# Optimization experiments

Measured on AMD Instinct MI355X. Metric: run time of the kernel, lower is better.

The kernel has to match this reference:

```python
import jax, jax.numpy as jnp
import numpy as np

B, S, D = 2, 2048, 1024
H = 16
HD = D // H  # 64


def setup_inputs() -> dict:
    key = jax.random.key(0)
    ks = jax.random.split(key, 6)
    sc = 1.0 / np.sqrt(D)
    x = jax.random.normal(ks[0], (B, S, D), dtype=jnp.float32)
    Wq = jax.random.normal(ks[1], (D, D), dtype=jnp.float32) * sc
    Wk = jax.random.normal(ks[2], (D, D), dtype=jnp.float32) * sc
    Wv = jax.random.normal(ks[3], (D, D), dtype=jnp.float32) * sc
    Wo = jax.random.normal(ks[4], (D, D), dtype=jnp.float32) * sc
    bo = jax.random.normal(ks[5], (D,), dtype=jnp.float32) * 0.01
    return {"x": x, "Wq": Wq, "Wk": Wk, "Wv": Wv, "Wo": Wo, "bo": bo}


def reference(x, Wq, Wk, Wv, Wo, bo):
    # projections: [B,S,D] -> [B,H,S,HD]
    def split_heads(t):
        return t.reshape(B, S, H, HD).transpose(0, 2, 1, 3)

    q = split_heads(x @ Wq)
    k = split_heads(x @ Wk)
    v = split_heads(x @ Wv)

    # naive full score matrix [B,H,S,S], masked causal, scaled softmax
    scores = jnp.einsum("bhqd,bhkd->bhqk", q, k)
    causal = jnp.tril(jnp.ones((S, S), dtype=bool))  # True = keep
    scores = jnp.where(causal, scores, -jnp.inf)
    attn = jax.nn.softmax(scores / np.sqrt(HD), axis=-1)

    ctx = jnp.einsum("bhqk,bhkd->bhqd", attn, v)  # [B,H,S,HD]
    ctx = ctx.transpose(0, 2, 1, 3).reshape(B, S, D)
    return ctx @ Wo + bo
```

## Files before the change

### kernel.cpp

```cpp
#include <hip/hip_runtime.h>

#define BB 2
#define SS 2048
#define DD 1024
#define HH 16
#define HD 64
#define MM (BB*SS)

typedef __bf16 bf16x8 __attribute__((ext_vector_type(8)));
typedef short  s16x4  __attribute__((ext_vector_type(4)));
typedef float  f32x4  __attribute__((ext_vector_type(4)));

#ifndef __has_builtin
#define __has_builtin(x) 0
#endif

__device__ __forceinline__ unsigned short f2bf(float f) {
    unsigned int u = __float_as_uint(f);
    u = (u + 0x7fffu + ((u >> 16) & 1u)) >> 16;
    return (unsigned short)u;
}
__device__ __forceinline__ unsigned int pack2(float a, float b) {
    return (unsigned int)f2bf(a) | ((unsigned int)f2bf(b) << 16);
}
__device__ __forceinline__ unsigned int pack2_fast(float a, float b) {
#if __has_builtin(__builtin_amdgcn_perm)
    return __builtin_amdgcn_perm(__float_as_uint(b) + 0x8000u,
                                 __float_as_uint(a) + 0x8000u, 0x07060302u);
#else
    return ((__float_as_uint(a) + 0x8000u) >> 16) |
           ((__float_as_uint(b) + 0x8000u) & 0xffff0000u);
#endif
}

__device__ __forceinline__ void gload_lds16(const unsigned short* g, unsigned short* l) {
    __builtin_amdgcn_global_load_lds(
        (const __attribute__((address_space(1))) void*)g,
        (__attribute__((address_space(3))) void*)l, 16, 0, 0);
}

__global__ __launch_bounds__(256) void prep_kernel(const float* __restrict__ x,
                                                   const float* __restrict__ Wq,
                                                   const float* __restrict__ Wk,
                                                   const float* __restrict__ Wv,
                                                   const float* __restrict__ Wo,
                                                   unsigned short* __restrict__ Xb,
                                                   unsigned short* __restrict__ Wqkvt,
                                                   unsigned short* __restrict__ Wot) {
    __shared__ float tile[32][33];
    const int bx = blockIdx.x;
    const int t = threadIdx.x;
    if (bx < 2048) {
        int gid = bx * 256 + t;
        int i = gid * 8;
        float4 a = *(const float4*)(x + i);
        float4 b = *(const float4*)(x + i + 4);
        uint4 o;
        o.x = pack2(a.x, a.y); o.y = pack2(a.z, a.w);
        o.z = pack2(b.x, b.y); o.w = pack2(b.z, b.w);
        ((uint4*)Xb)[gid] = o;
        return;
    }
    int pb = bx - 2048;
    int p = pb >> 10, rem = pb & 1023;
    int bxx = rem & 31, byy = rem >> 5;
    const float* src = (p == 0) ? Wq : (p == 1) ? Wk : (p == 2) ? Wv : Wo;
    unsigned short* dst = (p == 3) ? Wot : (Wqkvt + (size_t)p * DD * DD);
    int tx = t & 31, ty = t >> 5;
    int n = bxx * 32 + tx;
#pragma unroll
    for (int i = 0; i < 4; ++i) {
        int k = byy * 32 + ty + i * 8;
        tile[ty + i * 8][tx] = src[k * DD + n];
    }
    __syncthreads();
#pragma unroll
    for (int i = 0; i < 4; ++i) {
        int n2 = bxx * 32 + ty + i * 8;
        int k2 = byy * 32 + tx;
        dst[n2 * DD + k2] = f2bf(tile[tx][ty + i * 8]);
    }
}

#define GEMM_K_LOOP(Aglob, Bglob)                                                 \
    __shared__ unsigned short smem[128 * 132];                                    \
    unsigned short (*As)[64]  = (unsigned short(*)[64])smem;                      \
    unsigned short (*Bs)[64]  = (unsigned short(*)[64])(smem + 128 * 64);         \
    unsigned short (*Es)[132] = (unsigned short(*)[132])smem;                     \
    const int n0 = blockIdx.x * 128, m0 = blockIdx.y * 128;                       \
    const int t = threadIdx.x;                                                    \
    const int wave = t >> 6, lane = t & 63;                                       \
    const int wm = wave >> 1, wn = wave & 1;                                      \
    const int l15 = lane & 15, quad = lane >> 4;                                  \
    const int lr = lane >> 3, lg = (lane & 7);                                    \
    const int lc = (lg ^ lr) * 8;                    \
    f32x4 acc[4][4];                                                              \
    _Pragma("unroll") for (int i = 0; i < 4; ++i)                                 \
        _Pragma("unroll") for (int j = 0; j < 4; ++j) acc[i][j] = f32x4{0,0,0,0}; \
    for (int kt = 0; kt < 16; ++kt) {                                             \
        if (kt) __syncthreads();                                                  \
        _Pragma("unroll") for (int i = 0; i < 4; ++i) {                           \
            int row = wave * 32 + i * 8;                                          \
            gload_lds16(Aglob + (size_t)(m0 + row + lr) * DD + kt * 64 + lc, &As[row][0]); \
            gload_lds16(Bglob + (size_t)(n0 + row + lr) * DD + kt * 64 + lc, &Bs[row][0]); \
        }                                                                         \
        __syncthreads();                                                          \
        _Pragma("unroll") for (int kh = 0; kh < 2; ++kh) {                        \
            bf16x8 af[4], bfr[4];                                                 \
            _Pragma("unroll") for (int s = 0; s < 4; ++s)                         \
                af[s] = *(const bf16x8*)&As[wm * 64 + s * 16 + l15][((kh * 4 + quad) ^ (l15 & 7)) * 8]; \
            _Pragma("unroll") for (int s = 0; s < 4; ++s)                         \
                bfr[s] = *(const bf16x8*)&Bs[wn * 64 + s * 16 + l15][((kh * 4 + quad) ^ (l15 & 7)) * 8]; \
            _Pragma("unroll") for (int i = 0; i < 4; ++i)                         \
                _Pragma("unroll") for (int j = 0; j < 4; ++j)                     \
                    acc[i][j] = __builtin_amdgcn_mfma_f32_16x16x32_bf16(af[i], bfr[j], acc[i][j], 0, 0, 0); \
        }                                                                         \
    }                                                                             \
    __syncthreads();

__global__ __launch_bounds__(256) void qkv_gemm_kernel(const unsigned short* __restrict__ Xb,
                                                       const unsigned short* __restrict__ Wt,
                                                       unsigned short* __restrict__ Qg,
                                                       unsigned short* __restrict__ Kg,
                                                       unsigned short* __restrict__ Vt) {
    GEMM_K_LOOP(Xb, Wt)
    const int p = n0 >> 10;
    const float qs = (p == 0) ? 0.18033688011112042f : 1.0f;
    if (p < 2) {
#pragma unroll
        for (int sm = 0; sm < 4; ++sm)
#pragma unroll
            for (int sn = 0; sn < 4; ++sn)
#pragma unroll
                for (int i = 0; i < 4; ++i)
                    Es[wm * 64 + sm * 16 + quad * 4 + i][wn * 64 + sn * 16 + l15] = f2bf(acc[sm][sn][i] * qs);
    } else {
#pragma unroll
        for (int sm = 0; sm < 4; ++sm)
#pragma unroll
            for (int sn = 0; sn < 4; ++sn)
#pragma unroll
                for (int i = 0; i < 4; ++i)
                    Es[wn * 64 + sn * 16 + l15][wm * 64 + sm * 16 + quad * 4 + i] = f2bf(acc[sm][sn][i]);
    }
    __syncthreads();
    const int h0 = (n0 & 1023) >> 6;
    if (p < 2) {
        unsigned short* dst0 = p ? Kg : Qg;
        int ml = t >> 1, seg = t & 1;
        int gm = m0 + ml, b = gm >> 11, s = gm & 2047;
        unsigned short* dptr = dst0 + ((size_t)(b * HH + h0 + seg) * SS + s) * HD;
#pragma unroll
        for (int j = 0; j < 8; ++j)
            *(uint4*)(dptr + j * 8) = *(const uint4*)&Es[ml][seg * 64 + j * 8];
    } else {
        int nl = t >> 1, mh = t & 1;
        int h = h0 + (nl >> 6), hd = nl & 63;
        int b = m0 >> 11, s0 = (m0 & 2047) + mh * 64;
        unsigned short* dptr = Vt + ((size_t)(b * HH + h) * HD + hd) * SS + s0;
#pragma unroll
        for (int j = 0; j < 8; ++j)
            *(uint4*)(dptr + j * 8) = *(const uint4*)&Es[nl][mh * 64 + j * 8];
    }
}

__global__ __launch_bounds__(256) void out_gemm_kernel(const unsigned short* __restrict__ Ctxb,
                                                       const unsigned short* __restrict__ Wot,
                                                       const float* __restrict__ bo,
                                                       float* __restrict__ out) {
    GEMM_K_LOOP(Ctxb, Wot)
    (void)Es;
#pragma unroll
    for (int sn = 0; sn < 4; ++sn) {
        int gn = n0 + wn * 64 + sn * 16 + l15;
        float bias = bo[gn];
#pragma unroll
        for (int sm = 0; sm < 4; ++sm)
#pragma unroll
            for (int i = 0; i < 4; ++i) {
                int gm = m0 + wm * 64 + sm * 16 + quad * 4 + i;
                out[(size_t)gm * DD + gn] = acc[sm][sn][i] + bias;
            }
    }
}

__global__ __launch_bounds__(256) void attn_kernel(const unsigned short* __restrict__ Qg,
                                                   const unsigned short* __restrict__ Kg,
                                                   const unsigned short* __restrict__ Vt,
                                                   unsigned short* __restrict__ Ctxb) {
    __shared__ unsigned short Ks[2][128][64];
    __shared__ unsigned short Vs[2][64][128];

    const int bh = blockIdx.x;
    const int qt = (int)gridDim.y - 1 - (int)blockIdx.y;
    const int t = threadIdx.x;
    const int wave = t >> 6, lane = t & 63;
    const int l15 = lane & 15, quad = lane >> 4;
    const int q0 = qt * 64;
    const int qmax = q0 + 63;
    const int b = bh >> 4, h = bh & 15;

    const unsigned short* Qb = Qg + (size_t)bh * SS * HD;
    const unsigned short* Kb = Kg + (size_t)bh * SS * HD;
    const unsigned short* Vb = Vt + (size_t)bh * HD * SS;

    const int qrow = q0 + wave * 16 + l15;
    bf16x8 bq[2];
#pragma unroll
    for (int hh = 0; hh < 2; ++hh)
        bq[hh] = *(const bf16x8*)(Qb + (size_t)qrow * HD + hh * 32 + quad * 8);

    const int rloc = lane >> 3, pcl = lane & 7;
    const int vrl = lane >> 4, vgc = lane & 15;
    const unsigned short* ksrc[4];
    const unsigned short* vsrc[4];
#pragma unroll
    for (int j = 0; j < 4; ++j) {
        int krow = (wave * 4 + j) * 8 + rloc;
        ksrc[j] = Kb + (size_t)krow * HD + (pcl ^ rloc) * 8;
        int vrow = wave * 16 + j * 4 + vrl;
        vsrc[j] = Vb + (size_t)vrow * SS + (vgc ^ (vrow & 15)) * 8;
    }

    f32x4 acc[4] = {f32x4{0,0,0,0}, f32x4{0,0,0,0}, f32x4{0,0,0,0}, f32x4{0,0,0,0}};
    float l = 0.f;
    const int nkt = (qmax >> 7) + 1;

#pragma unroll
    for (int j = 0; j < 4; ++j) {
        gload_lds16(ksrc[j], &Ks[0][(wave * 4 + j) * 8][0]);
        gload_lds16(vsrc[j], &Vs[0][wave * 16 + j * 4][0]);
    }
    __syncthreads();

    for (int kt = 0; kt < nkt; ++kt) {
        const int buf = kt & 1;
        const int k0 = kt * 128;
        if (kt + 1 < nkt) {
            const int nb = buf ^ 1;
#pragma unroll
            for (int j = 0; j < 4; ++j) {
                gload_lds16(ksrc[j] + (size_t)(kt + 1) * 128 * HD, &Ks[nb][(wave * 4 + j) * 8][0]);
                gload_lds16(vsrc[j] + (kt + 1) * 128,              &Vs[nb][wave * 16 + j * 4][0]);
            }
        }

        auto tile_body = [&](int kbmax, bool tail) {
#pragma unroll
            for (int kb = 0; kb < 8; ++kb) {
                if (kb >= kbmax) continue;
                f32x4 St = f32x4{0, 0, 0, 0};
#pragma unroll
                for (int hh = 0; hh < 2; ++hh) {
                    bf16x8 ak = *(const bf16x8*)&Ks[buf][kb * 16 + l15][((hh * 4 + quad) ^ (l15 & 7)) * 8];
                    St = __builtin_amdgcn_mfma_f32_16x16x32_bf16(ak, bq[hh], St, 0, 0, 0);
                }
                if (tail) {
#pragma unroll
                    for (int r = 0; r < 4; ++r)
                        if (k0 + kb * 16 + quad * 4 + r > qrow) St[r] = -1e30f;
                }
                float e0 = __builtin_amdgcn_exp2f(St[0]);
                float e1 = __builtin_amdgcn_exp2f(St[1]);
                float e2 = __builtin_amdgcn_exp2f(St[2]);
                float e3 = __builtin_amdgcn_exp2f(St[3]);
                l += (e0 + e1) + (e2 + e3);
                uint2 uu;
                uu.x = pack2_fast(e0, e1);
                uu.y = pack2_fast(e2, e3);
                s16x4 ap = *(s16x4*)&uu;
#pragma unroll
                for (int db = 0; db < 4; ++db) {
                    const int pg = (2 * kb + (quad >> 1)) ^ l15;
                    s16x4 bv = *(const s16x4*)&Vs[buf][db * 16 + l15][pg * 8 + (quad & 1) * 4];
                    acc[db] = __builtin_amdgcn_mfma_f32_16x16x16bf16_1k(ap, bv, acc[db], 0, 0, 0);
                }
            }
        };
        if (kt == nkt - 1) tile_body(((qmax - k0) >> 4) + 1, true);
        else               tile_body(8, false);

        __syncthreads();
    }

    l += __shfl_xor(l, 16, 64);
    l += __shfl_xor(l, 32, 64);
    float linv = 1.0f / l;
#pragma unroll
    for (int r = 0; r < 4; ++r) {
        float ir = __shfl(linv, quad * 4 + r, 64);
        int gq = q0 + wave * 16 + quad * 4 + r;
        size_t base = ((size_t)(b * SS + gq)) * DD + h * HD;
#pragma unroll
        for (int db = 0; db < 4; ++db)
            Ctxb[base + db * 16 + l15] = f2bf(acc[db][r] * ir);
    }
}

extern "C" void kernel_launch(void* const* d_in, const int* in_sizes, int n_in,
                              void* d_out, int out_size, void* d_ws, size_t ws_size,
                              hipStream_t stream) {
    const float* x  = (const float*)d_in[0];
    const float* Wq = (const float*)d_in[1];
    const float* Wk = (const float*)d_in[2];
    const float* Wv = (const float*)d_in[3];
    const float* Wo = (const float*)d_in[4];
    const float* bo = (const float*)d_in[5];
    float* out = (float*)d_out;

    char* w = (char*)d_ws;
    unsigned short* Xb    = (unsigned short*)(w);
    unsigned short* Wqkvt = (unsigned short*)(w + (size_t)(8 << 20));
    unsigned short* Wot   = (unsigned short*)(w + (size_t)(14 << 20));
    unsigned short* Qg    = (unsigned short*)(w + (size_t)(16 << 20));
    unsigned short* Kg    = (unsigned short*)(w + (size_t)(24 << 20));
    unsigned short* Vt    = (unsigned short*)(w + (size_t)(32 << 20));
    unsigned short* Ctxb  = (unsigned short*)(w + (size_t)(40 << 20));

    prep_kernel<<<6144, 256, 0, stream>>>(x, Wq, Wk, Wv, Wo, Xb, Wqkvt, Wot);
    qkv_gemm_kernel<<<dim3(3 * DD / 128, MM / 128), 256, 0, stream>>>(Xb, Wqkvt, Qg, Kg, Vt);
    attn_kernel<<<dim3(BB * HH, SS / 64), 256, 0, stream>>>(Qg, Kg, Vt, Ctxb);
    out_gemm_kernel<<<dim3(DD / 128, MM / 128), 256, 0, stream>>>(Ctxb, Wot, bo, out);
}
```

Measured before the change: 174.1 us.

## Double query rows per attention block and compute row sums via MFMA

Each attention block now handles 128 query rows instead of 64, with every wave processing two 16-row query fragments that share each loaded K and V fragment from LDS. This halves K/V global-to-LDS traffic per query and amortizes the LDS reads. The softmax denominator is now accumulated with an MFMA against a ones vector instead of scalar adds plus cross-lane shuffles. In exchange the grid is halved, which reduces parallelism, and the diagonal tile no longer skips fully masked sub-blocks. Register pressure also rises.

```diff
diff --git a/kernel.cpp b/kernel.cpp
--- a/kernel.cpp
+++ b/kernel.cpp
@@ -196,19 +196,22 @@
     const int t = threadIdx.x;
     const int wave = t >> 6, lane = t & 63;
     const int l15 = lane & 15, quad = lane >> 4;
-    const int q0 = qt * 64;
-    const int qmax = q0 + 63;
+    const int q0 = qt * 128;
     const int b = bh >> 4, h = bh & 15;
 
     const unsigned short* Qb = Qg + (size_t)bh * SS * HD;
     const unsigned short* Kb = Kg + (size_t)bh * SS * HD;
     const unsigned short* Vb = Vt + (size_t)bh * HD * SS;
 
-    const int qrow = q0 + wave * 16 + l15;
-    bf16x8 bq[2];
-#pragma unroll
-    for (int hh = 0; hh < 2; ++hh)
-        bq[hh] = *(const bf16x8*)(Qb + (size_t)qrow * HD + hh * 32 + quad * 8);
+    int qrow[2];
+    bf16x8 bq[2][2];
+#pragma unroll
+    for (int qf = 0; qf < 2; ++qf) {
+        qrow[qf] = q0 + wave * 32 + qf * 16 + l15;
+#pragma unroll
+        for (int hh = 0; hh < 2; ++hh)
+            bq[qf][hh] = *(const bf16x8*)(Qb + (size_t)qrow[qf] * HD + hh * 32 + quad * 8);
+    }
 
     const int rloc = lane >> 3, pcl = lane & 7;
     const int vrl = lane >> 4, vgc = lane & 15;
@@ -222,9 +225,14 @@
         vsrc[j] = Vb + (size_t)vrow * SS + (vgc ^ (vrow & 15)) * 8;
     }
 
-    f32x4 acc[4] = {f32x4{0,0,0,0}, f32x4{0,0,0,0}, f32x4{0,0,0,0}, f32x4{0,0,0,0}};
-    float l = 0.f;
-    const int nkt = (qmax >> 7) + 1;
+    f32x4 acc[2][4];
+#pragma unroll
+    for (int qf = 0; qf < 2; ++qf)
+#pragma unroll
+        for (int db = 0; db < 4; ++db) acc[qf][db] = f32x4{0,0,0,0};
+    f32x4 accl[2] = {f32x4{0,0,0,0}, f32x4{0,0,0,0}};
+    const s16x4 ones = {(short)0x3F80, (short)0x3F80, (short)0x3F80, (short)0x3F80};
+    const int nkt = qt + 1;
 
 #pragma unroll
     for (int j = 0; j < 4; ++j) {
@@ -245,55 +253,60 @@
             }
         }
 
-        auto tile_body = [&](int kbmax, bool tail) {
-#pragma unroll
-            for (int kb = 0; kb < 8; ++kb) {
-                if (kb >= kbmax) continue;
-                f32x4 St = f32x4{0, 0, 0, 0};
-#pragma unroll
-                for (int hh = 0; hh < 2; ++hh) {
-                    bf16x8 ak = *(const bf16x8*)&Ks[buf][kb * 16 + l15][((hh * 4 + quad) ^ (l15 & 7)) * 8];
-                    St = __builtin_amdgcn_mfma_f32_16x16x32_bf16(ak, bq[hh], St, 0, 0, 0);
-                }
-                if (tail) {
+        const bool tail = (kt == nkt - 1);
+#pragma unroll
+        for (int kb = 0; kb < 8; ++kb) {
+            f32x4 St[2] = {f32x4{0,0,0,0}, f32x4{0,0,0,0}};
+#pragma unroll
+            for (int hh = 0; hh < 2; ++hh) {
+                bf16x8 ak = *(const bf16x8*)&Ks[buf][kb * 16 + l15][((hh * 4 + quad) ^ (l15 & 7)) * 8];
+                St[0] = __builtin_amdgcn_mfma_f32_16x16x32_bf16(ak, bq[0][hh], St[0], 0, 0, 0);
+                St[1] = __builtin_amdgcn_mfma_f32_16x16x32_bf16(ak, bq[1][hh], St[1], 0, 0, 0);
+            }
+            if (tail) {
+#pragma unroll
+                for (int qf = 0; qf < 2; ++qf)
 #pragma unroll
                     for (int r = 0; r < 4; ++r)
-                        if (k0 + kb * 16 + quad * 4 + r > qrow) St[r] = -1e30f;
-                }
-                float e0 = __builtin_amdgcn_exp2f(St[0]);
-                float e1 = __builtin_amdgcn_exp2f(St[1]);
-                float e2 = __builtin_amdgcn_exp2f(St[2]);
-                float e3 = __builtin_amdgcn_exp2f(St[3]);
-                l += (e0 + e1) + (e2 + e3);
+                        if (k0 + kb * 16 + quad * 4 + r > qrow[qf]) St[qf][r] = -1e30f;
+            }
+            s16x4 ap[2];
+#pragma unroll
+            for (int qf = 0; qf < 2; ++qf) {
+                float e0 = __builtin_amdgcn_exp2f(St[qf][0]);
+                float e1 = __builtin_amdgcn_exp2f(St[qf][1]);
+                float e2 = __builtin_amdgcn_exp2f(St[qf][2]);
+                float e3 = __builtin_amdgcn_exp2f(St[qf][3]);
                 uint2 uu;
                 uu.x = pack2_fast(e0, e1);
                 uu.y = pack2_fast(e2, e3);
-                s16x4 ap = *(s16x4*)&uu;
-#pragma unroll
-                for (int db = 0; db < 4; ++db) {
-                    const int pg = (2 * kb + (quad >> 1)) ^ l15;
-                    s16x4 bv = *(const s16x4*)&Vs[buf][db * 16 + l15][pg * 8 + (quad & 1) * 4];
-                    acc[db] = __builtin_amdgcn_mfma_f32_16x16x16bf16_1k(ap, bv, acc[db], 0, 0, 0);
-                }
-            }
-        };
-        if (kt == nkt - 1) tile_body(((qmax - k0) >> 4) + 1, true);
-        else               tile_body(8, false);
+                ap[qf] = *(s16x4*)&uu;
+            }
+#pragma unroll
+            for (int db = 0; db < 4; ++db) {
+                const int pg = (2 * kb + (quad >> 1)) ^ l15;
+                s16x4 bv = *(const s16x4*)&Vs[buf][db * 16 + l15][pg * 8 + (quad & 1) * 4];
+                acc[0][db] = __builtin_amdgcn_mfma_f32_16x16x16bf16_1k(ap[0], bv, acc[0][db], 0, 0, 0);
+                acc[1][db] = __builtin_amdgcn_mfma_f32_16x16x16bf16_1k(ap[1], bv, acc[1][db], 0, 0, 0);
+            }
+            accl[0] = __builtin_amdgcn_mfma_f32_16x16x16bf16_1k(ap[0], ones, accl[0], 0, 0, 0);
+            accl[1] = __builtin_amdgcn_mfma_f32_16x16x16bf16_1k(ap[1], ones, accl[1], 0, 0, 0);
+        }
 
         __syncthreads();
     }
 
-    l += __shfl_xor(l, 16, 64);
-    l += __shfl_xor(l, 32, 64);
-    float linv = 1.0f / l;
-#pragma unroll
-    for (int r = 0; r < 4; ++r) {
-        float ir = __shfl(linv, quad * 4 + r, 64);
-        int gq = q0 + wave * 16 + quad * 4 + r;
-        size_t base = ((size_t)(b * SS + gq)) * DD + h * HD;
-#pragma unroll
-        for (int db = 0; db < 4; ++db)
-            Ctxb[base + db * 16 + l15] = f2bf(acc[db][r] * ir);
+#pragma unroll
+    for (int qf = 0; qf < 2; ++qf) {
+#pragma unroll
+        for (int r = 0; r < 4; ++r) {
+            float ir = 1.0f / accl[qf][r];
+            int gq = q0 + wave * 32 + qf * 16 + quad * 4 + r;
+            size_t base = ((size_t)(b * SS + gq)) * DD + h * HD;
+#pragma unroll
+            for (int db = 0; db < 4; ++db)
+                Ctxb[base + db * 16 + l15] = f2bf(acc[qf][db][r] * ir);
+        }
     }
 }
 
@@ -319,6 +332,6 @@
 
     prep_kernel<<<6144, 256, 0, stream>>>(x, Wq, Wk, Wv, Wo, Xb, Wqkvt, Wot);
     qkv_gemm_kernel<<<dim3(3 * DD / 128, MM / 128), 256, 0, stream>>>(Xb, Wqkvt, Qg, Kg, Vt);
-    attn_kernel<<<dim3(BB * HH, SS / 64), 256, 0, stream>>>(Qg, Kg, Vt, Ctxb);
+    attn_kernel<<<dim3(BB * HH, SS / 128), 256, 0, stream>>>(Qg, Kg, Vt, Ctxb);
     out_gemm_kernel<<<dim3(DD / 128, MM / 128), 256, 0, stream>>>(Ctxb, Wot, bo, out);
 }
```

Result: slower. 178.6 us (+2.6%).
